# Performance work log

Hardware: AMD Instinct MI355X
Metric: run time of the kernel (lower is better)

## Reference

```python
import jax, jax.numpy as jnp
import numpy as np

B, LQ, LK = 16, 256, 256
DQ = DK = DV = H = 256


def setup_inputs() -> dict:
    key = jax.random.key(0)
    ks = jax.random.split(key, 7)
    queries = jax.random.normal(ks[0], (B, LQ, DQ), dtype=jnp.float32)
    keys = jax.random.normal(ks[1], (B, LK, DK), dtype=jnp.float32)
    values = jax.random.normal(ks[2], (B, LK, DV), dtype=jnp.float32)
    valid_lens = jax.random.randint(ks[3], (B,), 1, LK + 1).astype(jnp.int32)
    W_q = jax.random.normal(ks[4], (DQ, H), dtype=jnp.float32) / np.sqrt(DQ)
    W_k = jax.random.normal(ks[5], (DK, H), dtype=jnp.float32) / np.sqrt(DK)
    w_v = jax.random.normal(ks[6], (H,), dtype=jnp.float32) / np.sqrt(H)
    return {"queries": queries, "keys": keys, "values": values,
            "valid_lens": valid_lens, "W_q": W_q, "W_k": W_k, "w_v": w_v}


def reference(queries, keys, values, valid_lens, W_q, W_k, w_v):
    # Project queries and keys to the hidden size (no bias)
    q = jnp.einsum('bqd,dh->bqh', queries, W_q)          # (B, Lq, H)
    k = jnp.einsum('bkd,dh->bkh', keys, W_k)             # (B, Lk, H)
    # Broadcast-add, tanh, then contract with w_v -> scores (B, Lq, Lk)
    features = jnp.tanh(q[:, :, None, :] + k[:, None, :, :])  # (B, Lq, Lk, H)
    scores = jnp.einsum('bqkh,h->bqk', features, w_v)
    # Masked softmax over last axis: positions >= valid_len get -1e6
    mask = jnp.arange(scores.shape[-1]) < valid_lens[:, None, None]  # (B,1,Lk) bcast
    scores = jnp.where(mask, scores, jnp.float32(-1e6))
    attn = jax.nn.softmax(scores, axis=-1)
    # Dropout is identity at inference (training=False)
    return jnp.einsum('bqk,bkv->bqv', attn, values)      # (B, Lq, Dv)
```

## Files before the change

### kernel.cpp

```cpp
#include <hip/hip_runtime.h>

using bf16x8 = __attribute__((ext_vector_type(8))) __bf16;
using f32x4  = __attribute__((ext_vector_type(4))) float;
using f32x2  = __attribute__((ext_vector_type(2))) float;
using us8    = __attribute__((ext_vector_type(8))) unsigned short;

#define TWO_LOG2E 2.8853900817779268f
#define LOG2E 1.4426950408889634f

__device__ __forceinline__ unsigned short f2bf(float x) {
  unsigned int u = __float_as_uint(x);
  u = (u + 0x7fffu + ((u >> 16) & 1u)) >> 16;
  return (unsigned short)u;
}
__device__ __forceinline__ float bf2f(unsigned short h) {
  return __uint_as_float(((unsigned int)h) << 16);
}
__device__ __forceinline__ f32x2 pk_fma(f32x2 a, f32x2 b, f32x2 c) {
  return __builtin_elementwise_fma(a, b, c);
}

__global__ __launch_bounds__(256) void tcast_kernel(
    const float* __restrict__ Wq, const float* __restrict__ Wk,
    const float* __restrict__ vals, const float* __restrict__ wv,
    unsigned short* __restrict__ wt_hi, unsigned short* __restrict__ wt_lo,
    unsigned short* __restrict__ vt_hi, unsigned short* __restrict__ vt_lo,
    float* __restrict__ wv2, float* __restrict__ Wsum) {
  if (blockIdx.x == 0) {
    int t = threadIdx.x;
    wv2[t] = -2.0f * wv[t];
    if (t < 64) {
      float s = wv[t] + wv[t + 64] + wv[t + 128] + wv[t + 192];
#pragma unroll
      for (int off = 1; off < 64; off <<= 1) s += __shfl_xor(s, off, 64);
      if (t == 0) Wsum[0] = s;
    }
  }
  __shared__ float tile[32][33];
  int m = blockIdx.x >> 6;
  int ts = blockIdx.x & 63;
  int R0 = (ts >> 3) << 5, C0 = (ts & 7) << 5;
  const float* src = (m == 0) ? Wq : (m == 1) ? Wk : (vals + ((m - 2) << 16));
  int r = threadIdx.x >> 3, c4 = (threadIdx.x & 7) << 2;
  float4 v = *(const float4*)(src + (R0 + r) * 256 + C0 + c4);
  tile[r][c4] = v.x; tile[r][c4 + 1] = v.y; tile[r][c4 + 2] = v.z; tile[r][c4 + 3] = v.w;
  __syncthreads();
  float o0 = tile[c4 + 0][r], o1 = tile[c4 + 1][r];
  float o2 = tile[c4 + 2][r], o3 = tile[c4 + 3][r];
  unsigned short h0 = f2bf(o0), h1 = f2bf(o1), h2 = f2bf(o2), h3 = f2bf(o3);
  int base = ((m < 2) ? (m << 16) : ((m - 2) << 16)) + (C0 + r) * 256 + R0 + c4;
  unsigned short* dh = (m < 2) ? wt_hi : vt_hi;
  unsigned short* dl = (m < 2) ? wt_lo : vt_lo;
  *(ushort4*)(dh + base) = make_ushort4(h0, h1, h2, h3);
  *(ushort4*)(dl + base) = make_ushort4(f2bf(o0 - bf2f(h0)), f2bf(o1 - bf2f(h1)),
                                        f2bf(o2 - bf2f(h2)), f2bf(o3 - bf2f(h3)));
}

__global__ __launch_bounds__(256, 4) void proj_kernel(
    const float* __restrict__ q, const float* __restrict__ kk,
    const unsigned short* __restrict__ w_hi, const unsigned short* __restrict__ w_lo,
    float* __restrict__ R) {
  int wave = threadIdx.x >> 6, lane = threadIdx.x & 63;
  int mt = (blockIdx.x << 1) + (wave & 1);
  int m0 = mt << 4;
  int g = mt >> 8;
  int r = lane & 15, qd = lane >> 4;
  int row = m0 + r;
  const float* A = (g == 0) ? (q + row * 256) : (kk + (row - 4096) * 256);
  bf16x8 ah[8], al[8];
#pragma unroll
  for (int s = 0; s < 8; ++s) {
    const float* p = A + qd * 8 + s * 32;
    float4 f0 = *(const float4*)p;
    float4 f1 = *(const float4*)(p + 4);
    float fv[8] = {f0.x, f0.y, f0.z, f0.w, f1.x, f1.y, f1.z, f1.w};
#pragma unroll
    for (int j = 0; j < 8; ++j) {
      __bf16 h = (__bf16)fv[j];
      ah[s][j] = h;
      al[s][j] = (__bf16)(fv[j] - (float)h);
    }
  }
  int nbase = (blockIdx.y << 6) + ((wave >> 1) << 5);
#pragma unroll
  for (int tI = 0; tI < 2; ++tI) {
    int n0 = nbase + (tI << 4);
    int boff = (g << 16) + (n0 + r) * 256 + qd * 8;
    f32x4 acc = {0.f, 0.f, 0.f, 0.f};
#pragma unroll
    for (int s = 0; s < 8; ++s) {
      bf16x8 bh = *(const bf16x8*)(w_hi + boff + s * 32);
      bf16x8 bl = *(const bf16x8*)(w_lo + boff + s * 32);
      acc = __builtin_amdgcn_mfma_f32_16x16x32_bf16(ah[s], bh, acc, 0, 0, 0);
      acc = __builtin_amdgcn_mfma_f32_16x16x32_bf16(ah[s], bl, acc, 0, 0, 0);
      acc = __builtin_amdgcn_mfma_f32_16x16x32_bf16(al[s], bh, acc, 0, 0, 0);
    }
#pragma unroll
    for (int i = 0; i < 4; ++i) {
      float l = acc[i] * TWO_LOG2E;
      l = fminf(fmaxf(l, -27.f), 27.f);
      R[(m0 + qd * 4 + i) * 256 + n0 + r] = __builtin_amdgcn_exp2f(l);
    }
  }
}

__global__ __launch_bounds__(256, 8) void scores_kernel(
    const float* __restrict__ R, const float* __restrict__ wv2,
    const float* __restrict__ Wsum, float* __restrict__ sc) {
  __shared__ __align__(16) float rqs[32 * 76];
  __shared__ __align__(16) float rkT[64 * 34];
  const int t = threadIdx.x;
  const int b = blockIdx.z;
  const int q0 = blockIdx.x << 5;
  const int k0 = blockIdx.y << 5;
  const int qrow = (b << 8) + q0;
  const int krow = (b << 8) + k0;
  const int tq = t >> 4, tk = t & 15;
  const int sr = t >> 3, shb = (t & 7) << 3;
  f32x2 a0 = {0.f, 0.f}, a1 = {0.f, 0.f};

  for (int hc = 0; hc < 4; ++hc) {
    if (hc) __syncthreads();
    const float* gq = R + (qrow + sr) * 256 + (hc << 6) + shb;
    *(float4*)(rqs + sr * 76 + shb)     = *(const float4*)gq;
    *(float4*)(rqs + sr * 76 + shb + 4) = *(const float4*)(gq + 4);
    const float* gk = R + (1 << 20) + (krow + sr) * 256 + (hc << 6) + shb;
    float4 w0 = *(const float4*)gk, w1 = *(const float4*)(gk + 4);
    rkT[(shb + 0) * 34 + sr] = w0.x;  rkT[(shb + 1) * 34 + sr] = w0.y;
    rkT[(shb + 2) * 34 + sr] = w0.z;  rkT[(shb + 3) * 34 + sr] = w0.w;
    rkT[(shb + 4) * 34 + sr] = w1.x;  rkT[(shb + 5) * 34 + sr] = w1.y;
    rkT[(shb + 6) * 34 + sr] = w1.z;  rkT[(shb + 7) * 34 + sr] = w1.w;
    __syncthreads();
#pragma unroll 2
    for (int h = 0; h < 64; h += 4) {
      f32x4 qa = *(const f32x4*)(rqs + tq * 76 + h);
      f32x4 qb = *(const f32x4*)(rqs + (tq + 16) * 76 + h);
      f32x4 wm = *(const f32x4*)(wv2 + (hc << 6) + h);
#pragma unroll
      for (int j = 0; j < 4; ++j) {
        f32x2 rk = *(const f32x2*)(rkT + (h + j) * 34 + (tk << 1));
        f32x2 d0 = pk_fma(rk, (f32x2)(qa[j]), (f32x2)(1.0f));
        f32x2 d1 = pk_fma(rk, (f32x2)(qb[j]), (f32x2)(1.0f));
        f32x2 r0, r1;
        r0.x = __uint_as_float(0x7EF311C3u - __float_as_uint(d0.x));
        r0.y = __uint_as_float(0x7EF311C3u - __float_as_uint(d0.y));
        r1.x = __uint_as_float(0x7EF311C3u - __float_as_uint(d1.x));
        r1.y = __uint_as_float(0x7EF311C3u - __float_as_uint(d1.y));
        r0 = r0 * pk_fma(-d0, r0, (f32x2)(2.0f));
        r1 = r1 * pk_fma(-d1, r1, (f32x2)(2.0f));
        f32x2 wj = (f32x2)(wm[j]);
        a0 = pk_fma(r0, wj, a0);
        a1 = pk_fma(r1, wj, a1);
      }
    }
  }
  float ws = Wsum[0];
  a0 += (f32x2)(ws);
  a1 += (f32x2)(ws);
  *(f32x2*)(sc + ((qrow + tq) << 8) + k0 + (tk << 1)) = a0;
  *(f32x2*)(sc + ((qrow + tq + 16) << 8) + k0 + (tk << 1)) = a1;
}

__global__ __launch_bounds__(256) void av_fused_kernel(
    const float* __restrict__ sc, const int* __restrict__ vlens,
    const unsigned short* __restrict__ vhi, const unsigned short* __restrict__ vlo,
    float* __restrict__ out) {
  __shared__ __align__(16) unsigned short athi[16 * 264];
  __shared__ __align__(16) unsigned short atlo[16 * 264];
  const int wave = threadIdx.x >> 6, lane = threadIdx.x & 63;
  const int m0 = blockIdx.x << 4;
  const int nh = blockIdx.y;
  const int b = blockIdx.z;
  const int vl = vlens[b];

  {
    int row = (wave << 2) + (lane & 3);
    int c0 = (lane >> 2) << 4;
    const float* srow = sc + ((b << 8) + m0 + row) * 256 + c0;
    float4 x0 = *(const float4*)(srow);
    float4 x1 = *(const float4*)(srow + 4);
    float4 x2 = *(const float4*)(srow + 8);
    float4 x3 = *(const float4*)(srow + 12);
    float p[16] = {x0.x, x0.y, x0.z, x0.w, x1.x, x1.y, x1.z, x1.w,
                   x2.x, x2.y, x2.z, x2.w, x3.x, x3.y, x3.z, x3.w};
#pragma unroll
    for (int i = 0; i < 16; ++i)
      if (c0 + i >= vl) p[i] = -1e6f;
    float mx = p[0];
#pragma unroll
    for (int i = 1; i < 16; ++i) mx = fmaxf(mx, p[i]);
#pragma unroll
    for (int off = 4; off <= 32; off <<= 1) mx = fmaxf(mx, __shfl_xor(mx, off, 64));
    float sm = 0.f;
#pragma unroll
    for (int i = 0; i < 16; ++i) {
      p[i] = __builtin_amdgcn_exp2f((p[i] - mx) * LOG2E);
      sm += p[i];
    }
#pragma unroll
    for (int off = 4; off <= 32; off <<= 1) sm += __shfl_xor(sm, off, 64);
    float rs = __builtin_amdgcn_rcpf(sm);
    us8 vh[2], vlo2[2];
#pragma unroll
    for (int i = 0; i < 16; ++i) {
      float sv = p[i] * rs;
      unsigned short h = f2bf(sv);
      vh[i >> 3][i & 7] = h;
      vlo2[i >> 3][i & 7] = f2bf(sv - bf2f(h));
    }
    *(us8*)(athi + row * 264 + c0)     = vh[0];
    *(us8*)(athi + row * 264 + c0 + 8) = vh[1];
    *(us8*)(atlo + row * 264 + c0)     = vlo2[0];
    *(us8*)(atlo + row * 264 + c0 + 8) = vlo2[1];
  }
  __syncthreads();

  const int r = lane & 15, qd = lane >> 4;
  bf16x8 ah[8], al[8];
#pragma unroll
  for (int s = 0; s < 8; ++s) {
    ah[s] = *(const bf16x8*)(athi + r * 264 + qd * 8 + s * 32);
    al[s] = *(const bf16x8*)(atlo + r * 264 + qd * 8 + s * 32);
  }
#pragma unroll
  for (int tI = 0; tI < 2; ++tI) {
    int n0 = (nh << 7) + (wave << 5) + (tI << 4);
    int boff = (b << 16) + (n0 + r) * 256 + qd * 8;
    f32x4 acc = {0.f, 0.f, 0.f, 0.f};
#pragma unroll
    for (int s = 0; s < 8; ++s) {
      bf16x8 bh = *(const bf16x8*)(vhi + boff + s * 32);
      bf16x8 bl = *(const bf16x8*)(vlo + boff + s * 32);
      acc = __builtin_amdgcn_mfma_f32_16x16x32_bf16(ah[s], bh, acc, 0, 0, 0);
      acc = __builtin_amdgcn_mfma_f32_16x16x32_bf16(ah[s], bl, acc, 0, 0, 0);
      acc = __builtin_amdgcn_mfma_f32_16x16x32_bf16(al[s], bh, acc, 0, 0, 0);
    }
#pragma unroll
    for (int i = 0; i < 4; ++i)
      out[(b << 16) + (m0 + qd * 4 + i) * 256 + n0 + r] = acc[i];
  }
}

extern "C" void kernel_launch(void* const* d_in, const int* in_sizes, int n_in,
                              void* d_out, int out_size, void* d_ws, size_t ws_size,
                              hipStream_t stream) {
  const float* queries = (const float*)d_in[0];
  const float* keys    = (const float*)d_in[1];
  const float* values  = (const float*)d_in[2];
  const int*   vlens   = (const int*)d_in[3];
  const float* Wq      = (const float*)d_in[4];
  const float* Wk      = (const float*)d_in[5];
  const float* wv      = (const float*)d_in[6];
  float* out = (float*)d_out;
  char* ws = (char*)d_ws;

  unsigned short* wt_hi = (unsigned short*)(ws + 0);
  unsigned short* wt_lo = (unsigned short*)(ws + 262144);
  unsigned short* vt_hi = (unsigned short*)(ws + 524288);
  unsigned short* vt_lo = (unsigned short*)(ws + 2621440);
  float*          R     = (float*)(ws + 4718592);
  float*          sc    = (float*)(ws + 13107200);
  float*          wv2   = (float*)(ws + 17301504);
  float*          Wsum  = (float*)(ws + 17302528);

  tcast_kernel<<<1152, 256, 0, stream>>>(Wq, Wk, values, wv,
                                         wt_hi, wt_lo, vt_hi, vt_lo, wv2, Wsum);
  proj_kernel<<<dim3(256, 4), 256, 0, stream>>>(queries, keys, wt_hi, wt_lo, R);
  scores_kernel<<<dim3(8, 8, 16), 256, 0, stream>>>(R, wv2, Wsum, sc);
  av_fused_kernel<<<dim3(16, 2, 16), 256, 0, stream>>>(sc, vlens, vt_hi, vt_lo, out);
}
```

Before: 138.7 us.

## Skip masked key positions across projection, scores and attention-value kernels

Uses valid_lens to skip work on key rows beyond each batch's valid length. The key projection waves exit early for those rows, scores blocks for fully masked key tiles return without writing, and the AV loop stops at the last 32-key slab that holds valid keys. The scores kernel is also retiled to 64 query rows per block, so each loaded key tile is reused across more queries, with the occupancy hint changed to match. The attention weights lose their low bf16 correction term, which removes one MFMA per step and a shared buffer but reduces the precision of the probabilities.

```diff
diff --git a/kernel.cpp b/kernel.cpp
--- a/kernel.cpp
+++ b/kernel.cpp
@@ -59,11 +59,15 @@
 __global__ __launch_bounds__(256, 4) void proj_kernel(
     const float* __restrict__ q, const float* __restrict__ kk,
     const unsigned short* __restrict__ w_hi, const unsigned short* __restrict__ w_lo,
-    float* __restrict__ R) {
+    const int* __restrict__ vlens, float* __restrict__ R) {
   int wave = threadIdx.x >> 6, lane = threadIdx.x & 63;
   int mt = (blockIdx.x << 1) + (wave & 1);
   int m0 = mt << 4;
   int g = mt >> 8;
+  if (g) {
+    int bb = (m0 >> 8) & 15;
+    if ((m0 & 255) >= vlens[bb]) return;
+  }
   int r = lane & 15, qd = lane >> 4;
   int row = m0 + r;
   const float* A = (g == 0) ? (q + row * 256) : (kk + (row - 4096) * 256);
@@ -104,61 +108,69 @@
   }
 }
 
-__global__ __launch_bounds__(256, 8) void scores_kernel(
+__global__ __launch_bounds__(256, 4) void scores_kernel(
     const float* __restrict__ R, const float* __restrict__ wv2,
-    const float* __restrict__ Wsum, float* __restrict__ sc) {
-  __shared__ __align__(16) float rqs[32 * 76];
-  __shared__ __align__(16) float rkT[64 * 34];
+    const float* __restrict__ Wsum, const int* __restrict__ vlens,
+    float* __restrict__ sc) {
+  const int b = blockIdx.z;
+  const int k0 = blockIdx.x << 5;
+  const int vl = vlens[b];
+  if (k0 >= vl) return;
+  __shared__ __align__(16) float qs[64 * 72];
+  __shared__ __align__(16) float kT[64 * 34];
   const int t = threadIdx.x;
-  const int b = blockIdx.z;
-  const int q0 = blockIdx.x << 5;
-  const int k0 = blockIdx.y << 5;
+  const int q0 = blockIdx.y << 6;
   const int qrow = (b << 8) + q0;
   const int krow = (b << 8) + k0;
   const int tq = t >> 4, tk = t & 15;
+  const int qr = t >> 2, qh = (t & 3) << 4;
   const int sr = t >> 3, shb = (t & 7) << 3;
-  f32x2 a0 = {0.f, 0.f}, a1 = {0.f, 0.f};
+  f32x2 acc[4] = {{0.f, 0.f}, {0.f, 0.f}, {0.f, 0.f}, {0.f, 0.f}};
 
   for (int hc = 0; hc < 4; ++hc) {
     if (hc) __syncthreads();
-    const float* gq = R + (qrow + sr) * 256 + (hc << 6) + shb;
-    *(float4*)(rqs + sr * 76 + shb)     = *(const float4*)gq;
-    *(float4*)(rqs + sr * 76 + shb + 4) = *(const float4*)(gq + 4);
+    const float* gq = R + (qrow + qr) * 256 + (hc << 6) + qh;
+    *(float4*)(qs + qr * 72 + qh)      = *(const float4*)(gq);
+    *(float4*)(qs + qr * 72 + qh + 4)  = *(const float4*)(gq + 4);
+    *(float4*)(qs + qr * 72 + qh + 8)  = *(const float4*)(gq + 8);
+    *(float4*)(qs + qr * 72 + qh + 12) = *(const float4*)(gq + 12);
     const float* gk = R + (1 << 20) + (krow + sr) * 256 + (hc << 6) + shb;
     float4 w0 = *(const float4*)gk, w1 = *(const float4*)(gk + 4);
-    rkT[(shb + 0) * 34 + sr] = w0.x;  rkT[(shb + 1) * 34 + sr] = w0.y;
-    rkT[(shb + 2) * 34 + sr] = w0.z;  rkT[(shb + 3) * 34 + sr] = w0.w;
-    rkT[(shb + 4) * 34 + sr] = w1.x;  rkT[(shb + 5) * 34 + sr] = w1.y;
-    rkT[(shb + 6) * 34 + sr] = w1.z;  rkT[(shb + 7) * 34 + sr] = w1.w;
+    kT[(shb + 0) * 34 + sr] = w0.x;  kT[(shb + 1) * 34 + sr] = w0.y;
+    kT[(shb + 2) * 34 + sr] = w0.z;  kT[(shb + 3) * 34 + sr] = w0.w;
+    kT[(shb + 4) * 34 + sr] = w1.x;  kT[(shb + 5) * 34 + sr] = w1.y;
+    kT[(shb + 6) * 34 + sr] = w1.z;  kT[(shb + 7) * 34 + sr] = w1.w;
     __syncthreads();
 #pragma unroll 2
     for (int h = 0; h < 64; h += 4) {
-      f32x4 qa = *(const f32x4*)(rqs + tq * 76 + h);
-      f32x4 qb = *(const f32x4*)(rqs + (tq + 16) * 76 + h);
+      f32x4 qv0 = *(const f32x4*)(qs + (tq +  0) * 72 + h);
+      f32x4 qv1 = *(const f32x4*)(qs + (tq + 16) * 72 + h);
+      f32x4 qv2 = *(const f32x4*)(qs + (tq + 32) * 72 + h);
+      f32x4 qv3 = *(const f32x4*)(qs + (tq + 48) * 72 + h);
       f32x4 wm = *(const f32x4*)(wv2 + (hc << 6) + h);
 #pragma unroll
       for (int j = 0; j < 4; ++j) {
-        f32x2 rk = *(const f32x2*)(rkT + (h + j) * 34 + (tk << 1));
-        f32x2 d0 = pk_fma(rk, (f32x2)(qa[j]), (f32x2)(1.0f));
-        f32x2 d1 = pk_fma(rk, (f32x2)(qb[j]), (f32x2)(1.0f));
-        f32x2 r0, r1;
-        r0.x = __uint_as_float(0x7EF311C3u - __float_as_uint(d0.x));
-        r0.y = __uint_as_float(0x7EF311C3u - __float_as_uint(d0.y));
-        r1.x = __uint_as_float(0x7EF311C3u - __float_as_uint(d1.x));
-        r1.y = __uint_as_float(0x7EF311C3u - __float_as_uint(d1.y));
-        r0 = r0 * pk_fma(-d0, r0, (f32x2)(2.0f));
-        r1 = r1 * pk_fma(-d1, r1, (f32x2)(2.0f));
+        f32x2 rk = *(const f32x2*)(kT + (h + j) * 34 + (tk << 1));
         f32x2 wj = (f32x2)(wm[j]);
-        a0 = pk_fma(r0, wj, a0);
-        a1 = pk_fma(r1, wj, a1);
+        float qj[4] = {qv0[j], qv1[j], qv2[j], qv3[j]};
+#pragma unroll
+        for (int i = 0; i < 4; ++i) {
+          f32x2 d = pk_fma(rk, (f32x2)(qj[i]), (f32x2)(1.0f));
+          f32x2 rr;
+          rr.x = __uint_as_float(0x7EF311C3u - __float_as_uint(d.x));
+          rr.y = __uint_as_float(0x7EF311C3u - __float_as_uint(d.y));
+          rr = rr * pk_fma(-d, rr, (f32x2)(2.0f));
+          acc[i] = pk_fma(rr, wj, acc[i]);
+        }
       }
     }
   }
   float ws = Wsum[0];
-  a0 += (f32x2)(ws);
-  a1 += (f32x2)(ws);
-  *(f32x2*)(sc + ((qrow + tq) << 8) + k0 + (tk << 1)) = a0;
-  *(f32x2*)(sc + ((qrow + tq + 16) << 8) + k0 + (tk << 1)) = a1;
+#pragma unroll
+  for (int i = 0; i < 4; ++i) {
+    f32x2 v = acc[i] + (f32x2)(ws);
+    *(f32x2*)(sc + ((qrow + tq + (i << 4)) << 8) + k0 + (tk << 1)) = v;
+  }
 }
 
 __global__ __launch_bounds__(256) void av_fused_kernel(
@@ -166,7 +178,6 @@
     const unsigned short* __restrict__ vhi, const unsigned short* __restrict__ vlo,
     float* __restrict__ out) {
   __shared__ __align__(16) unsigned short athi[16 * 264];
-  __shared__ __align__(16) unsigned short atlo[16 * 264];
   const int wave = threadIdx.x >> 6, lane = threadIdx.x & 63;
   const int m0 = blockIdx.x << 4;
   const int nh = blockIdx.y;
@@ -200,40 +211,27 @@
 #pragma unroll
     for (int off = 4; off <= 32; off <<= 1) sm += __shfl_xor(sm, off, 64);
     float rs = __builtin_amdgcn_rcpf(sm);
-    us8 vh[2], vlo2[2];
-#pragma unroll
-    for (int i = 0; i < 16; ++i) {
-      float sv = p[i] * rs;
-      unsigned short h = f2bf(sv);
-      vh[i >> 3][i & 7] = h;
-      vlo2[i >> 3][i & 7] = f2bf(sv - bf2f(h));
-    }
+    us8 vh[2];
+#pragma unroll
+    for (int i = 0; i < 16; ++i) vh[i >> 3][i & 7] = f2bf(p[i] * rs);
     *(us8*)(athi + row * 264 + c0)     = vh[0];
     *(us8*)(athi + row * 264 + c0 + 8) = vh[1];
-    *(us8*)(atlo + row * 264 + c0)     = vlo2[0];
-    *(us8*)(atlo + row * 264 + c0 + 8) = vlo2[1];
   }
   __syncthreads();
 
   const int r = lane & 15, qd = lane >> 4;
-  bf16x8 ah[8], al[8];
-#pragma unroll
-  for (int s = 0; s < 8; ++s) {
-    ah[s] = *(const bf16x8*)(athi + r * 264 + qd * 8 + s * 32);
-    al[s] = *(const bf16x8*)(atlo + r * 264 + qd * 8 + s * 32);
-  }
+  const int smax = (vl + 31) >> 5;
 #pragma unroll
   for (int tI = 0; tI < 2; ++tI) {
     int n0 = (nh << 7) + (wave << 5) + (tI << 4);
     int boff = (b << 16) + (n0 + r) * 256 + qd * 8;
     f32x4 acc = {0.f, 0.f, 0.f, 0.f};
-#pragma unroll
-    for (int s = 0; s < 8; ++s) {
+    for (int s = 0; s < smax; ++s) {
+      bf16x8 ah = *(const bf16x8*)(athi + r * 264 + qd * 8 + s * 32);
       bf16x8 bh = *(const bf16x8*)(vhi + boff + s * 32);
       bf16x8 bl = *(const bf16x8*)(vlo + boff + s * 32);
-      acc = __builtin_amdgcn_mfma_f32_16x16x32_bf16(ah[s], bh, acc, 0, 0, 0);
-      acc = __builtin_amdgcn_mfma_f32_16x16x32_bf16(ah[s], bl, acc, 0, 0, 0);
-      acc = __builtin_amdgcn_mfma_f32_16x16x32_bf16(al[s], bh, acc, 0, 0, 0);
+      acc = __builtin_amdgcn_mfma_f32_16x16x32_bf16(ah, bh, acc, 0, 0, 0);
+      acc = __builtin_amdgcn_mfma_f32_16x16x32_bf16(ah, bl, acc, 0, 0, 0);
     }
 #pragma unroll
     for (int i = 0; i < 4; ++i)
@@ -265,7 +263,7 @@
 
   tcast_kernel<<<1152, 256, 0, stream>>>(Wq, Wk, values, wv,
                                          wt_hi, wt_lo, vt_hi, vt_lo, wv2, Wsum);
-  proj_kernel<<<dim3(256, 4), 256, 0, stream>>>(queries, keys, wt_hi, wt_lo, R);
-  scores_kernel<<<dim3(8, 8, 16), 256, 0, stream>>>(R, wv2, Wsum, sc);
+  proj_kernel<<<dim3(256, 4), 256, 0, stream>>>(queries, keys, wt_hi, wt_lo, vlens, R);
+  scores_kernel<<<dim3(8, 4, 16), 256, 0, stream>>>(R, wv2, Wsum, vlens, sc);
   av_fused_kernel<<<dim3(16, 2, 16), 256, 0, stream>>>(sc, vlens, vt_hi, vt_lo, out);
 }
```

Measured after the change: 139.0 us. No clear change (+0.2%).

## Skip masked key blocks, store K projection transposed, drop low-part of attention weights

Applied to the files above, without the earlier changes.

The projection kernel skips key tiles beyond each batch's valid length and writes the key projection transposed, so the scores kernel loads it with contiguous float4 reads instead of a scattered LDS transpose. The scores kernel exits early for key blocks past the valid length. The attention-times-values kernel limits its MFMA loop to the valid key range and drops the bf16 low-part correction of the attention weights, which removes a third of the MFMAs but lowers the precision of the attention weights. Unwritten score columns past the valid length are read but masked before the softmax, and the grid order is changed so blocks of the same batch are adjacent.

```diff
diff --git a/kernel.cpp b/kernel.cpp
--- a/kernel.cpp
+++ b/kernel.cpp
@@ -59,11 +59,15 @@
 __global__ __launch_bounds__(256, 4) void proj_kernel(
     const float* __restrict__ q, const float* __restrict__ kk,
     const unsigned short* __restrict__ w_hi, const unsigned short* __restrict__ w_lo,
-    float* __restrict__ R) {
+    const int* __restrict__ vlens, float* __restrict__ Rq, float* __restrict__ RkT) {
   int wave = threadIdx.x >> 6, lane = threadIdx.x & 63;
   int mt = (blockIdx.x << 1) + (wave & 1);
   int m0 = mt << 4;
   int g = mt >> 8;
+  if (g) {
+    int bb = (m0 >> 8) & 15;
+    if ((m0 & 255) >= vlens[bb]) return;
+  }
   int r = lane & 15, qd = lane >> 4;
   int row = m0 + r;
   const float* A = (g == 0) ? (q + row * 256) : (kk + (row - 4096) * 256);
@@ -95,41 +99,51 @@
       acc = __builtin_amdgcn_mfma_f32_16x16x32_bf16(ah[s], bl, acc, 0, 0, 0);
       acc = __builtin_amdgcn_mfma_f32_16x16x32_bf16(al[s], bh, acc, 0, 0, 0);
     }
+    f32x4 ex;
 #pragma unroll
     for (int i = 0; i < 4; ++i) {
       float l = acc[i] * TWO_LOG2E;
       l = fminf(fmaxf(l, -27.f), 27.f);
-      R[(m0 + qd * 4 + i) * 256 + n0 + r] = __builtin_amdgcn_exp2f(l);
+      ex[i] = __builtin_amdgcn_exp2f(l);
+    }
+    if (g == 0) {
+#pragma unroll
+      for (int i = 0; i < 4; ++i)
+        Rq[(m0 + qd * 4 + i) * 256 + n0 + r] = ex[i];
+    } else {
+      int b = (m0 >> 8) & 15;
+      int kloc = (m0 & 255) + qd * 4;
+      *(f32x4*)(RkT + (b << 16) + (n0 + r) * 256 + kloc) = ex;
     }
   }
 }
 
 __global__ __launch_bounds__(256, 8) void scores_kernel(
-    const float* __restrict__ R, const float* __restrict__ wv2,
-    const float* __restrict__ Wsum, float* __restrict__ sc) {
+    const float* __restrict__ Rq, const float* __restrict__ RkT,
+    const float* __restrict__ wv2, const float* __restrict__ Wsum,
+    const int* __restrict__ vlens, float* __restrict__ sc) {
+  const int b = blockIdx.x;
+  const int k0 = blockIdx.y << 5;
+  const int vl = vlens[b];
+  if (k0 >= vl) return;
   __shared__ __align__(16) float rqs[32 * 76];
-  __shared__ __align__(16) float rkT[64 * 34];
+  __shared__ __align__(16) float kT[64 * 34];
   const int t = threadIdx.x;
-  const int b = blockIdx.z;
-  const int q0 = blockIdx.x << 5;
-  const int k0 = blockIdx.y << 5;
+  const int q0 = blockIdx.z << 5;
   const int qrow = (b << 8) + q0;
-  const int krow = (b << 8) + k0;
   const int tq = t >> 4, tk = t & 15;
   const int sr = t >> 3, shb = (t & 7) << 3;
+  const int hrow = t >> 2, kq = (t & 3) << 3;
   f32x2 a0 = {0.f, 0.f}, a1 = {0.f, 0.f};
 
   for (int hc = 0; hc < 4; ++hc) {
     if (hc) __syncthreads();
-    const float* gq = R + (qrow + sr) * 256 + (hc << 6) + shb;
+    const float* gq = Rq + (qrow + sr) * 256 + (hc << 6) + shb;
     *(float4*)(rqs + sr * 76 + shb)     = *(const float4*)gq;
     *(float4*)(rqs + sr * 76 + shb + 4) = *(const float4*)(gq + 4);
-    const float* gk = R + (1 << 20) + (krow + sr) * 256 + (hc << 6) + shb;
-    float4 w0 = *(const float4*)gk, w1 = *(const float4*)(gk + 4);
-    rkT[(shb + 0) * 34 + sr] = w0.x;  rkT[(shb + 1) * 34 + sr] = w0.y;
-    rkT[(shb + 2) * 34 + sr] = w0.z;  rkT[(shb + 3) * 34 + sr] = w0.w;
-    rkT[(shb + 4) * 34 + sr] = w1.x;  rkT[(shb + 5) * 34 + sr] = w1.y;
-    rkT[(shb + 6) * 34 + sr] = w1.z;  rkT[(shb + 7) * 34 + sr] = w1.w;
+    const float* gk = RkT + (b << 16) + ((hc << 6) + hrow) * 256 + k0 + kq;
+    *(float4*)(kT + hrow * 34 + kq)     = *(const float4*)gk;
+    *(float4*)(kT + hrow * 34 + kq + 4) = *(const float4*)(gk + 4);
     __syncthreads();
 #pragma unroll 2
     for (int h = 0; h < 64; h += 4) {
@@ -138,7 +152,8 @@
       f32x4 wm = *(const f32x4*)(wv2 + (hc << 6) + h);
 #pragma unroll
       for (int j = 0; j < 4; ++j) {
-        f32x2 rk = *(const f32x2*)(rkT + (h + j) * 34 + (tk << 1));
+        f32x2 rk = *(const f32x2*)(kT + (h + j) * 34 + (tk << 1));
+        f32x2 wj = (f32x2)(wm[j]);
         f32x2 d0 = pk_fma(rk, (f32x2)(qa[j]), (f32x2)(1.0f));
         f32x2 d1 = pk_fma(rk, (f32x2)(qb[j]), (f32x2)(1.0f));
         f32x2 r0, r1;
@@ -148,7 +163,6 @@
         r1.y = __uint_as_float(0x7EF311C3u - __float_as_uint(d1.y));
         r0 = r0 * pk_fma(-d0, r0, (f32x2)(2.0f));
         r1 = r1 * pk_fma(-d1, r1, (f32x2)(2.0f));
-        f32x2 wj = (f32x2)(wm[j]);
         a0 = pk_fma(r0, wj, a0);
         a1 = pk_fma(r1, wj, a1);
       }
@@ -166,11 +180,10 @@
     const unsigned short* __restrict__ vhi, const unsigned short* __restrict__ vlo,
     float* __restrict__ out) {
   __shared__ __align__(16) unsigned short athi[16 * 264];
-  __shared__ __align__(16) unsigned short atlo[16 * 264];
   const int wave = threadIdx.x >> 6, lane = threadIdx.x & 63;
-  const int m0 = blockIdx.x << 4;
+  const int b = blockIdx.x;
   const int nh = blockIdx.y;
-  const int b = blockIdx.z;
+  const int m0 = blockIdx.z << 4;
   const int vl = vlens[b];
 
   {
@@ -200,40 +213,27 @@
 #pragma unroll
     for (int off = 4; off <= 32; off <<= 1) sm += __shfl_xor(sm, off, 64);
     float rs = __builtin_amdgcn_rcpf(sm);
-    us8 vh[2], vlo2[2];
-#pragma unroll
-    for (int i = 0; i < 16; ++i) {
-      float sv = p[i] * rs;
-      unsigned short h = f2bf(sv);
-      vh[i >> 3][i & 7] = h;
-      vlo2[i >> 3][i & 7] = f2bf(sv - bf2f(h));
-    }
+    us8 vh[2];
+#pragma unroll
+    for (int i = 0; i < 16; ++i) vh[i >> 3][i & 7] = f2bf(p[i] * rs);
     *(us8*)(athi + row * 264 + c0)     = vh[0];
     *(us8*)(athi + row * 264 + c0 + 8) = vh[1];
-    *(us8*)(atlo + row * 264 + c0)     = vlo2[0];
-    *(us8*)(atlo + row * 264 + c0 + 8) = vlo2[1];
   }
   __syncthreads();
 
   const int r = lane & 15, qd = lane >> 4;
-  bf16x8 ah[8], al[8];
-#pragma unroll
-  for (int s = 0; s < 8; ++s) {
-    ah[s] = *(const bf16x8*)(athi + r * 264 + qd * 8 + s * 32);
-    al[s] = *(const bf16x8*)(atlo + r * 264 + qd * 8 + s * 32);
-  }
+  const int smax = (vl + 31) >> 5;
 #pragma unroll
   for (int tI = 0; tI < 2; ++tI) {
     int n0 = (nh << 7) + (wave << 5) + (tI << 4);
     int boff = (b << 16) + (n0 + r) * 256 + qd * 8;
     f32x4 acc = {0.f, 0.f, 0.f, 0.f};
-#pragma unroll
-    for (int s = 0; s < 8; ++s) {
+    for (int s = 0; s < smax; ++s) {
+      bf16x8 ah = *(const bf16x8*)(athi + r * 264 + qd * 8 + s * 32);
       bf16x8 bh = *(const bf16x8*)(vhi + boff + s * 32);
       bf16x8 bl = *(const bf16x8*)(vlo + boff + s * 32);
-      acc = __builtin_amdgcn_mfma_f32_16x16x32_bf16(ah[s], bh, acc, 0, 0, 0);
-      acc = __builtin_amdgcn_mfma_f32_16x16x32_bf16(ah[s], bl, acc, 0, 0, 0);
-      acc = __builtin_amdgcn_mfma_f32_16x16x32_bf16(al[s], bh, acc, 0, 0, 0);
+      acc = __builtin_amdgcn_mfma_f32_16x16x32_bf16(ah, bh, acc, 0, 0, 0);
+      acc = __builtin_amdgcn_mfma_f32_16x16x32_bf16(ah, bl, acc, 0, 0, 0);
     }
 #pragma unroll
     for (int i = 0; i < 4; ++i)
@@ -258,14 +258,16 @@
   unsigned short* wt_lo = (unsigned short*)(ws + 262144);
   unsigned short* vt_hi = (unsigned short*)(ws + 524288);
   unsigned short* vt_lo = (unsigned short*)(ws + 2621440);
-  float*          R     = (float*)(ws + 4718592);
+  float*          Rq    = (float*)(ws + 4718592);
+  float*          RkT   = (float*)(ws + 8912896);
   float*          sc    = (float*)(ws + 13107200);
   float*          wv2   = (float*)(ws + 17301504);
   float*          Wsum  = (float*)(ws + 17302528);
 
   tcast_kernel<<<1152, 256, 0, stream>>>(Wq, Wk, values, wv,
                                          wt_hi, wt_lo, vt_hi, vt_lo, wv2, Wsum);
-  proj_kernel<<<dim3(256, 4), 256, 0, stream>>>(queries, keys, wt_hi, wt_lo, R);
-  scores_kernel<<<dim3(8, 8, 16), 256, 0, stream>>>(R, wv2, Wsum, sc);
+  proj_kernel<<<dim3(256, 4), 256, 0, stream>>>(queries, keys, wt_hi, wt_lo,
+                                                vlens, Rq, RkT);
+  scores_kernel<<<dim3(16, 8, 8), 256, 0, stream>>>(Rq, RkT, wv2, Wsum, vlens, sc);
   av_fused_kernel<<<dim3(16, 2, 16), 256, 0, stream>>>(sc, vlens, vt_hi, vt_lo, out);
 }
```

Measured after the change: 139.4 us. Within noise of the previous version (+0.5%).
